# Kernel tuning notes

Measured on AMD Instinct MI355X. Metric: run time of the kernel, lower is better.

The kernel has to match this reference:

```python
import jax, jax.numpy as jnp
import numpy as np

N = 100000   # nodes
E = 1600000  # edges (avg degree 16)
F_IN, F_HID, F_OUT = 64, 64, 16


def setup_inputs() -> dict:
    key = jax.random.key(0)
    ks = jax.random.split(key, 10)
    features = jax.random.normal(ks[0], (N, F_IN), dtype=jnp.float32)
    src = jax.random.randint(ks[1], (E,), 0, N, dtype=jnp.int32)
    dst = jax.random.randint(ks[2], (E,), 0, N, dtype=jnp.int32)
    # Xavier-uniform weights, zero bias (matches nn.init in the module)
    def xavier(k, fan_in, fan_out):
        lim = np.sqrt(6.0 / (fan_in + fan_out))
        return jax.random.uniform(k, (fan_in, fan_out), jnp.float32, -lim, lim)
    return {
        "features": features,
        "W1": xavier(ks[3], F_IN, F_HID), "b1": jnp.zeros((F_HID,), jnp.float32),
        "W2": xavier(ks[4], F_HID, F_HID), "b2": jnp.zeros((F_HID,), jnp.float32),
        "W3": xavier(ks[5], F_HID, F_OUT), "b3": jnp.zeros((F_OUT,), jnp.float32),
        "src": src, "dst": dst,
    }


def pairnorm_scs(x):
    # PairNorm 'PN-SCS', scale=1
    col_mean = x.mean(axis=0)                                    # [F]
    rownorm = jnp.sqrt(1e-6 + jnp.sum(x * x, axis=1, keepdims=True))  # [N,1]
    return x / rownorm - col_mean


def graph_conv(h, src, dst, W, b):
    # copy_u('h','m') + sum reduce over edges, plus self-loop
    agg = jax.ops.segment_sum(h[src], dst, num_segments=N) + h   # [N,F]
    return agg @ W + b


def reference(features, W1, b1, W2, b2, W3, b3, src, dst):
    h = features
    for W, b in ((W1, b1), (W2, b2)):
        h = pairnorm_scs(h)
        h = jax.nn.relu(graph_conv(h, src, dst, W, b))
        # dropout p=0.0 -> identity
    return graph_conv(h, src, dst, W3, b3)
```

## Files before the change

kernel.cpp:

```cpp
#include <hip/hip_runtime.h>
#include <hip/hip_fp8.h>


#define NHB 128

__device__ __forceinline__ unsigned short f2bf(float f) {
  unsigned u = __builtin_bit_cast(unsigned, f);
  u += 0x7FFFu + ((u >> 16) & 1u);
  return (unsigned short)(u >> 16);
}
__device__ __forceinline__ float bf2f(unsigned short h) {
  return __builtin_bit_cast(float, ((unsigned)h) << 16);
}
__device__ __forceinline__ float rlane(float v, int k) {
  return __builtin_bit_cast(
      float, __builtin_amdgcn_readlane(__builtin_bit_cast(int, v), k));
}
__device__ __forceinline__ unsigned char f2fp8(float f) {
  __hip_fp8_e4m3 t(f);
  return (unsigned char)t.__x;
}
__device__ __forceinline__ float fp8tof(unsigned v) {
#if __has_builtin(__builtin_amdgcn_cvt_f32_fp8)
  return __builtin_amdgcn_cvt_f32_fp8((int)v, 0);
#else
  const unsigned h = ((v << 8) & 0x8000u) | ((v << 7) & 0x3f80u);
  __half_raw hr; hr.x = (unsigned short)h;
  return (float)__half(hr) * 256.0f;
#endif
}

__global__ __launch_bounds__(256) void prelude_kernel(
    const int* __restrict__ dst, int* __restrict__ cntA, int E,
    const float* __restrict__ x, float* __restrict__ cs, int n4) {
  __shared__ int lc[NHB];
  __shared__ float lds[16][64];
  const int t = threadIdx.x;
  if (t < NHB) lc[t] = 0;
  __syncthreads();
  const int stride = gridDim.x * blockDim.x;
  for (int e = blockIdx.x * blockDim.x + t; e < E; e += stride)
    atomicAdd(&lc[__builtin_nontemporal_load(&dst[e]) >> 10], 1);

  float s0 = 0.f, s1 = 0.f, s2 = 0.f, s3 = 0.f;
  for (int i = blockIdx.x * blockDim.x + t; i < n4; i += stride) {
    float4 v = ((const float4*)x)[i];
    s0 += v.x; s1 += v.y; s2 += v.z; s3 += v.w;
  }
  const int r = t >> 4;
  const int cq = (t & 15) * 4;
  lds[r][cq + 0] = s0; lds[r][cq + 1] = s1; lds[r][cq + 2] = s2; lds[r][cq + 3] = s3;
  __syncthreads();
  if (t < NHB && lc[t]) atomicAdd(&cntA[t], lc[t]);
  if (t < 64) {
    float tot = 0.f;
    #pragma unroll
    for (int rr = 0; rr < 16; ++rr) tot += lds[rr][t];
    unsafeAtomicAdd(&cs[t], tot);
  }
}

__global__ void colsum_kernel(const float* __restrict__ x, float* __restrict__ cs,
                              int n4) {
  __shared__ float lds[16][64];
  float s0 = 0.f, s1 = 0.f, s2 = 0.f, s3 = 0.f;
  const int t = threadIdx.x;
  const int stride = gridDim.x * blockDim.x;
  for (int i = blockIdx.x * blockDim.x + t; i < n4; i += stride) {
    float4 v = ((const float4*)x)[i];
    s0 += v.x; s1 += v.y; s2 += v.z; s3 += v.w;
  }
  const int r = t >> 4;
  const int cq = (t & 15) * 4;
  lds[r][cq + 0] = s0; lds[r][cq + 1] = s1; lds[r][cq + 2] = s2; lds[r][cq + 3] = s3;
  __syncthreads();
  if (t < 64) {
    float tot = 0.f;
    #pragma unroll
    for (int rr = 0; rr < 16; ++rr) tot += lds[rr][t];
    unsafeAtomicAdd(&cs[t], tot);
  }
}

__global__ __launch_bounds__(256) void matnorm_kernel(
    const float* x, const float* __restrict__ W,
    const float* __restrict__ cs, unsigned char* __restrict__ z,
    int N, float invN) {
  const int lane = threadIdx.x & 63;
  const int wid  = blockIdx.x * (blockDim.x >> 6) + (threadIdx.x >> 6);
  const int nw   = gridDim.x * (blockDim.x >> 6);

  float w[64];
  float cm0 = 0.f, cm1 = 0.f, cm2 = 0.f, cm3 = 0.f;
  #pragma unroll
  for (int k = 0; k < 64; k += 4) {
    w[k + 0] = W[(k + 0) * 64 + lane];
    w[k + 1] = W[(k + 1) * 64 + lane];
    w[k + 2] = W[(k + 2) * 64 + lane];
    w[k + 3] = W[(k + 3) * 64 + lane];
    cm0 = fmaf(cs[k + 0], w[k + 0], cm0);
    cm1 = fmaf(cs[k + 1], w[k + 1], cm1);
    cm2 = fmaf(cs[k + 2], w[k + 2], cm2);
    cm3 = fmaf(cs[k + 3], w[k + 3], cm3);
  }
  const float cm = ((cm0 + cm1) + (cm2 + cm3)) * invN;

  for (int row = wid; row < N; row += nw) {
    const float xv = x[(size_t)row * 64 + lane];
    float ss = xv * xv;
    #pragma unroll
    for (int m = 1; m < 64; m <<= 1) ss += __shfl_xor(ss, m, 64);
    const float rinv = 1.0f / sqrtf(1e-6f + ss);
    float a0 = 0.f, a1 = 0.f, a2 = 0.f, a3 = 0.f;
    #pragma unroll
    for (int k = 0; k < 64; k += 4) {
      a0 = fmaf(rlane(xv, k + 0), w[k + 0], a0);
      a1 = fmaf(rlane(xv, k + 1), w[k + 1], a1);
      a2 = fmaf(rlane(xv, k + 2), w[k + 2], a2);
      a3 = fmaf(rlane(xv, k + 3), w[k + 3], a3);
    }
    const float acc = (a0 + a1) + (a2 + a3);
    z[(size_t)row * 64 + lane] = f2fp8(acc * rinv - cm);
  }
}


__global__ void scanA_kernel(const int* __restrict__ cntA,
                             int* __restrict__ baseA, int* __restrict__ curA,
                             int NHI) {
  if (threadIdx.x == 0) {
    int acc = 0;
    for (int p = 0; p < NHI; ++p) { baseA[p] = acc; curA[p] = acc; acc += cntA[p]; }
    baseA[NHI] = acc;
  }
}

#define TILE 2048
#define CAPA 48
__global__ __launch_bounds__(256) void scatterA_kernel(
    const int* __restrict__ src, const int* __restrict__ dst,
    int* __restrict__ curA, unsigned* __restrict__ ppack, int E) {
  __shared__ unsigned lpk[NHB][CAPA];
  __shared__ int lcnt[NHB], lbase[NHB];
  const int t = threadIdx.x;
  if (t < NHB) lcnt[t] = 0;
  __syncthreads();
  const int ntiles = (E + TILE - 1) / TILE;
  for (int tile = blockIdx.x; tile < ntiles; tile += gridDim.x) {
    const int base = tile * TILE;
    #pragma unroll
    for (int j = 0; j < TILE / 256; ++j) {
      const int e = base + j * 256 + t;
      if (e < E) {
        const int d = __builtin_nontemporal_load(&dst[e]);
        const int s = __builtin_nontemporal_load(&src[e]);
        const unsigned pw = ((unsigned)s << 10) | ((unsigned)d & 1023u);
        const int p = d >> 10;
        const int slot = atomicAdd(&lcnt[p], 1);
        if (slot < CAPA) lpk[p][slot] = pw;
        else ppack[atomicAdd(&curA[p], 1)] = pw;
      }
    }
    __syncthreads();
    if (t < NHB) {
      int c = lcnt[t]; if (c > CAPA) c = CAPA;
      lbase[t] = c ? atomicAdd(&curA[t], c) : 0;
      lcnt[t] = c;
    }
    __syncthreads();
    for (int p = 0; p < NHB; ++p) {
      const int c = lcnt[p];
      if (t < c) ppack[lbase[p] + t] = lpk[p][t];
    }
    __syncthreads();
    if (t < NHB) lcnt[t] = 0;
    __syncthreads();
  }
}

__global__ __launch_bounds__(1024) void fillsort_kernel(
    const unsigned* __restrict__ ppack, const int* __restrict__ baseA,
    int* __restrict__ rowstart, int* __restrict__ csr, int N, int E) {
  __shared__ int hist[1024];
  __shared__ int bs[1024];
  const int t = threadIdx.x;
  const int h = blockIdx.x;
  const int nlo = h << 10;
  const int elo = baseA[h], ehi = baseA[h + 1];

  hist[t] = 0;
  __syncthreads();

  int e = elo + t;
  for (; e + 3 * 1024 < ehi; e += 4 * 1024) {
    const unsigned p0 = ppack[e], p1 = ppack[e + 1024],
                   p2 = ppack[e + 2048], p3 = ppack[e + 3072];
    atomicAdd(&hist[p0 & 1023u], 1); atomicAdd(&hist[p1 & 1023u], 1);
    atomicAdd(&hist[p2 & 1023u], 1); atomicAdd(&hist[p3 & 1023u], 1);
  }
  for (; e < ehi; e += 1024) atomicAdd(&hist[ppack[e] & 1023u], 1);
  __syncthreads();

  const int c = hist[t];
  bs[t] = c;
  __syncthreads();
  for (int off = 1; off < 1024; off <<= 1) {
    const int v = (t >= off) ? bs[t - off] : 0;
    __syncthreads();
    bs[t] += v;
    __syncthreads();
  }
  const int excl = bs[t] - c;

  hist[t] = excl;
  const int n0 = nlo + t;
  if (n0 < N) rowstart[n0] = elo + excl;
  if (h == 0 && t == 0) rowstart[N] = E;
  __syncthreads();

  e = elo + t;
  for (; e + 3 * 1024 < ehi; e += 4 * 1024) {
    const unsigned p0 = ppack[e],        p1 = ppack[e + 1024];
    const unsigned p2 = ppack[e + 2048], p3 = ppack[e + 3072];
    csr[elo + atomicAdd(&hist[p0 & 1023u], 1)] = (int)(p0 >> 10);
    csr[elo + atomicAdd(&hist[p1 & 1023u], 1)] = (int)(p1 >> 10);
    csr[elo + atomicAdd(&hist[p2 & 1023u], 1)] = (int)(p2 >> 10);
    csr[elo + atomicAdd(&hist[p3 & 1023u], 1)] = (int)(p3 >> 10);
  }
  for (; e < ehi; e += 1024) {
    const unsigned p = ppack[e];
    csr[elo + atomicAdd(&hist[p & 1023u], 1)] = (int)(p >> 10);
  }
}

__global__ __launch_bounds__(256) void gather64_kernel(
    const unsigned char* __restrict__ z, const float* __restrict__ b,
    const int* __restrict__ rowstart, const int* __restrict__ csr,
    float* __restrict__ agg, int N) {
  const int lane = threadIdx.x & 63;
  int node = blockIdx.x * (blockDim.x >> 6) + (threadIdx.x >> 6);
  if (node >= N) return;
  node = __builtin_amdgcn_readfirstlane(node);
  const int start = rowstart[node];
  const int end   = rowstart[node + 1];
  const unsigned char hs = z[(size_t)node * 64 + lane];
  float a0 = 0.f, a1 = 0.f, a2 = 0.f, a3 = 0.f;
  int e = start;
  for (; e + 16 <= end; e += 16) {
    unsigned char h[16];
    #pragma unroll
    for (int j = 0; j < 16; ++j) h[j] = z[(size_t)csr[e + j] * 64 + lane];
    #pragma unroll
    for (int j = 0; j < 16; j += 4) {
      a0 += fp8tof(h[j + 0]); a1 += fp8tof(h[j + 1]);
      a2 += fp8tof(h[j + 2]); a3 += fp8tof(h[j + 3]);
    }
  }
  for (; e + 4 <= end; e += 4) {
    unsigned char h[4];
    #pragma unroll
    for (int j = 0; j < 4; ++j) h[j] = z[(size_t)csr[e + j] * 64 + lane];
    a0 += fp8tof(h[0]); a1 += fp8tof(h[1]); a2 += fp8tof(h[2]); a3 += fp8tof(h[3]);
  }
  for (; e < end; ++e) a0 += fp8tof(z[(size_t)csr[e] * 64 + lane]);
  const float sum = (a0 + a1) + (a2 + a3);
  agg[(size_t)node * 64 + lane] = fmaxf(fp8tof(hs) + b[lane] + sum, 0.f);
}

__global__ __launch_bounds__(256) void gather_l2_kernel(
    const unsigned char* __restrict__ z2, const float* __restrict__ b2,
    const float* __restrict__ W3, const int* __restrict__ rowstart,
    const int* __restrict__ csr, unsigned short* __restrict__ z3, int N) {
  const int lane = threadIdx.x & 63;
  int node = blockIdx.x * (blockDim.x >> 6) + (threadIdx.x >> 6);
  if (node >= N) return;
  node = __builtin_amdgcn_readfirstlane(node);
  float4 w4[4];
  #pragma unroll
  for (int q = 0; q < 4; ++q)
    w4[q] = ((const float4*)(W3 + lane * 16))[q];

  const int start = rowstart[node];
  const int end   = rowstart[node + 1];
  const unsigned char hs = z2[(size_t)node * 64 + lane];
  float a0 = 0.f, a1 = 0.f, a2 = 0.f, a3 = 0.f;
  int e = start;
  for (; e + 16 <= end; e += 16) {
    unsigned char h[16];
    #pragma unroll
    for (int j = 0; j < 16; ++j) h[j] = z2[(size_t)csr[e + j] * 64 + lane];
    #pragma unroll
    for (int j = 0; j < 16; j += 4) {
      a0 += fp8tof(h[j + 0]); a1 += fp8tof(h[j + 1]);
      a2 += fp8tof(h[j + 2]); a3 += fp8tof(h[j + 3]);
    }
  }
  for (; e + 4 <= end; e += 4) {
    unsigned char h[4];
    #pragma unroll
    for (int j = 0; j < 4; ++j) h[j] = z2[(size_t)csr[e + j] * 64 + lane];
    a0 += fp8tof(h[0]); a1 += fp8tof(h[1]); a2 += fp8tof(h[2]); a3 += fp8tof(h[3]);
  }
  for (; e < end; ++e) a0 += fp8tof(z2[(size_t)csr[e] * 64 + lane]);
  const float sum = (a0 + a1) + (a2 + a3);
  const float o = fmaxf(fp8tof(hs) + b2[lane] + sum, 0.f);

  float p[16];
  #pragma unroll
  for (int q = 0; q < 4; ++q) {
    p[4 * q + 0] = o * w4[q].x;
    p[4 * q + 1] = o * w4[q].y;
    p[4 * q + 2] = o * w4[q].z;
    p[4 * q + 3] = o * w4[q].w;
  }
  {
    const bool up = (lane & 1);
    #pragma unroll
    for (int m = 0; m < 8; ++m) {
      const float mine = up ? p[m + 8] : p[m];
      const float give = up ? p[m] : p[m + 8];
      p[m] = mine + __shfl_xor(give, 1, 64);
    }
  }
  {
    const bool up = (lane & 2);
    #pragma unroll
    for (int m = 0; m < 4; ++m) {
      const float mine = up ? p[m + 4] : p[m];
      const float give = up ? p[m] : p[m + 4];
      p[m] = mine + __shfl_xor(give, 2, 64);
    }
  }
  {
    const bool up = (lane & 4);
    #pragma unroll
    for (int m = 0; m < 2; ++m) {
      const float mine = up ? p[m + 2] : p[m];
      const float give = up ? p[m] : p[m + 2];
      p[m] = mine + __shfl_xor(give, 4, 64);
    }
  }
  {
    const bool up = (lane & 8);
    const float mine = up ? p[1] : p[0];
    const float give = up ? p[0] : p[1];
    p[0] = mine + __shfl_xor(give, 8, 64);
  }
  p[0] += __shfl_xor(p[0], 16, 64);
  p[0] += __shfl_xor(p[0], 32, 64);

  if (lane < 16) {
    const int j = ((lane & 1) << 3) | ((lane & 2) << 1) |
                  ((lane & 4) >> 1) | ((lane & 8) >> 3);
    z3[(size_t)node * 16 + j] = f2bf(p[0]);
  }
}

__global__ __launch_bounds__(256) void gather16_kernel(
    const unsigned short* __restrict__ z3, const float* __restrict__ b3,
    const int* __restrict__ rowstart, const int* __restrict__ csr,
    float* __restrict__ out, int N) {
  const int lane = threadIdx.x & 63;
  const int f = lane & 15;
  const int g = lane >> 4;
  int node = blockIdx.x * (blockDim.x >> 6) + (threadIdx.x >> 6);
  if (node >= N) return;
  node = __builtin_amdgcn_readfirstlane(node);
  const int start = rowstart[node];
  const int end   = rowstart[node + 1];
  float acc0 = 0.f, acc1 = 0.f;
  int e = start + g;
  for (; e + 4 < end; e += 8) {
    acc0 += bf2f(z3[(size_t)csr[e] * 16 + f]);
    acc1 += bf2f(z3[(size_t)csr[e + 4] * 16 + f]);
  }
  if (e < end) acc0 += bf2f(z3[(size_t)csr[e] * 16 + f]);
  float acc = acc0 + acc1;
  acc += __shfl_xor(acc, 16, 64);
  acc += __shfl_xor(acc, 32, 64);
  if (lane < 16)
    out[(size_t)node * 16 + f] = bf2f(z3[(size_t)node * 16 + f]) + b3[f] + acc;
}

extern "C" void kernel_launch(void* const* d_in, const int* in_sizes, int n_in,
                              void* d_out, int out_size, void* d_ws, size_t ws_size,
                              hipStream_t stream) {
  const float* feat = (const float*)d_in[0];
  const float* W1 = (const float*)d_in[1];
  const float* b1 = (const float*)d_in[2];
  const float* W2 = (const float*)d_in[3];
  const float* b2 = (const float*)d_in[4];
  const float* W3 = (const float*)d_in[5];
  const float* b3 = (const float*)d_in[6];
  const int* src = (const int*)d_in[7];
  const int* dst = (const int*)d_in[8];
  const int N = in_sizes[0] / 64;
  const int E = in_sizes[7];
  float* out = (float*)d_out;

  float* B            = (float*)d_ws;
  unsigned char* zb   = (unsigned char*)(B + (size_t)N * 64);
  unsigned short* z3b = (unsigned short*)(zb + (size_t)N * 64);
  int* cntA  = (int*)(z3b + (size_t)N * 16);
  float* cs1 = (float*)(cntA + NHB);
  float* cs2 = cs1 + 64;
  int* baseA    = (int*)(cs2 + 64);
  int* curA     = baseA + NHB + 1;
  int* rowstart = curA + NHB;
  int* csr      = rowstart + N + 1;
  unsigned* ppack = (unsigned*)zb;

  const int NHI = (N + 1023) >> 10;
  const int node_blocks = (N + 3) / 4;
  const float invN = 1.0f / (float)N;

  hipMemsetAsync(cntA, 0, (NHB + 128) * sizeof(int), stream);
  prelude_kernel<<<512, 256, 0, stream>>>(dst, cntA, E, feat, cs1, N * 16);
  scanA_kernel<<<1, 64, 0, stream>>>(cntA, baseA, curA, NHI);
  scatterA_kernel<<<512, 256, 0, stream>>>(src, dst, curA, ppack, E);
  fillsort_kernel<<<NHI, 1024, 0, stream>>>(ppack, baseA, rowstart, csr, N, E);

  matnorm_kernel<<<1024, 256, 0, stream>>>(feat, W1, cs1, zb, N, invN);
  gather64_kernel<<<node_blocks, 256, 0, stream>>>(zb, b1, rowstart, csr, B, N);

  colsum_kernel<<<512, 256, 0, stream>>>(B, cs2, N * 16);
  matnorm_kernel<<<1024, 256, 0, stream>>>(B, W2, cs2, zb, N, invN);
  gather_l2_kernel<<<node_blocks, 256, 0, stream>>>(zb, b2, W3, rowstart, csr,
                                                    z3b, N);

  gather16_kernel<<<node_blocks, 256, 0, stream>>>(z3b, b3, rowstart, csr, out, N);
}
```

Before: 394.3 us.

## Fuse column sum into layer-1 gather, parallel bucket scan, fp8 final features

Layer 1's gather becomes a grid-stride kernel that also accumulates per-column sums of its ReLU output and adds them atomically. This removes the separate colsum pass over the N×64 float buffer. The single-thread bucket scan becomes a 128-thread shared-memory Hillis-Steele scan. The 16-wide layer-3 projected features are stored as fp8 instead of bf16, halving gather16's read traffic at the cost of precision.

```diff
diff --git a/kernel.cpp b/kernel.cpp
--- a/kernel.cpp
+++ b/kernel.cpp
@@ -52,28 +52,6 @@
   lds[r][cq + 0] = s0; lds[r][cq + 1] = s1; lds[r][cq + 2] = s2; lds[r][cq + 3] = s3;
   __syncthreads();
   if (t < NHB && lc[t]) atomicAdd(&cntA[t], lc[t]);
-  if (t < 64) {
-    float tot = 0.f;
-    #pragma unroll
-    for (int rr = 0; rr < 16; ++rr) tot += lds[rr][t];
-    unsafeAtomicAdd(&cs[t], tot);
-  }
-}
-
-__global__ void colsum_kernel(const float* __restrict__ x, float* __restrict__ cs,
-                              int n4) {
-  __shared__ float lds[16][64];
-  float s0 = 0.f, s1 = 0.f, s2 = 0.f, s3 = 0.f;
-  const int t = threadIdx.x;
-  const int stride = gridDim.x * blockDim.x;
-  for (int i = blockIdx.x * blockDim.x + t; i < n4; i += stride) {
-    float4 v = ((const float4*)x)[i];
-    s0 += v.x; s1 += v.y; s2 += v.z; s3 += v.w;
-  }
-  const int r = t >> 4;
-  const int cq = (t & 15) * 4;
-  lds[r][cq + 0] = s0; lds[r][cq + 1] = s1; lds[r][cq + 2] = s2; lds[r][cq + 3] = s3;
-  __syncthreads();
   if (t < 64) {
     float tot = 0.f;
     #pragma unroll
@@ -128,11 +106,22 @@
 __global__ void scanA_kernel(const int* __restrict__ cntA,
                              int* __restrict__ baseA, int* __restrict__ curA,
                              int NHI) {
-  if (threadIdx.x == 0) {
-    int acc = 0;
-    for (int p = 0; p < NHI; ++p) { baseA[p] = acc; curA[p] = acc; acc += cntA[p]; }
-    baseA[NHI] = acc;
-  }
+  __shared__ int s[NHB];
+  const int t = threadIdx.x;
+  const int v = (t < NHI) ? cntA[t] : 0;
+  s[t] = v;
+  __syncthreads();
+  int acc = v;
+  for (int off = 1; off < NHB; off <<= 1) {
+    const int add = (t >= off) ? s[t - off] : 0;
+    __syncthreads();
+    acc += add;
+    s[t] = acc;
+    __syncthreads();
+  }
+  const int excl = acc - v;
+  if (t < NHI) { baseA[t] = excl; curA[t] = excl; }
+  if (t == NHI - 1) baseA[NHI] = acc;
 }
 
 #define TILE 2048
@@ -236,41 +225,54 @@
 __global__ __launch_bounds__(256) void gather64_kernel(
     const unsigned char* __restrict__ z, const float* __restrict__ b,
     const int* __restrict__ rowstart, const int* __restrict__ csr,
-    float* __restrict__ agg, int N) {
+    float* __restrict__ agg, float* __restrict__ cs, int N) {
+  __shared__ float lred[4][64];
   const int lane = threadIdx.x & 63;
-  int node = blockIdx.x * (blockDim.x >> 6) + (threadIdx.x >> 6);
-  if (node >= N) return;
-  node = __builtin_amdgcn_readfirstlane(node);
-  const int start = rowstart[node];
-  const int end   = rowstart[node + 1];
-  const unsigned char hs = z[(size_t)node * 64 + lane];
-  float a0 = 0.f, a1 = 0.f, a2 = 0.f, a3 = 0.f;
-  int e = start;
-  for (; e + 16 <= end; e += 16) {
-    unsigned char h[16];
-    #pragma unroll
-    for (int j = 0; j < 16; ++j) h[j] = z[(size_t)csr[e + j] * 64 + lane];
-    #pragma unroll
-    for (int j = 0; j < 16; j += 4) {
-      a0 += fp8tof(h[j + 0]); a1 += fp8tof(h[j + 1]);
-      a2 += fp8tof(h[j + 2]); a3 += fp8tof(h[j + 3]);
-    }
-  }
-  for (; e + 4 <= end; e += 4) {
-    unsigned char h[4];
-    #pragma unroll
-    for (int j = 0; j < 4; ++j) h[j] = z[(size_t)csr[e + j] * 64 + lane];
-    a0 += fp8tof(h[0]); a1 += fp8tof(h[1]); a2 += fp8tof(h[2]); a3 += fp8tof(h[3]);
-  }
-  for (; e < end; ++e) a0 += fp8tof(z[(size_t)csr[e] * 64 + lane]);
-  const float sum = (a0 + a1) + (a2 + a3);
-  agg[(size_t)node * 64 + lane] = fmaxf(fp8tof(hs) + b[lane] + sum, 0.f);
+  const int wv   = threadIdx.x >> 6;
+  const int nw   = gridDim.x * (blockDim.x >> 6);
+  const float bl = b[lane];
+  float csum = 0.f;
+  for (int node = blockIdx.x * (blockDim.x >> 6) + wv; node < N; node += nw) {
+    const int n = __builtin_amdgcn_readfirstlane(node);
+    const int start = rowstart[n];
+    const int end   = rowstart[n + 1];
+    const unsigned char hs = z[(size_t)n * 64 + lane];
+    float a0 = 0.f, a1 = 0.f, a2 = 0.f, a3 = 0.f;
+    int e = start;
+    for (; e + 16 <= end; e += 16) {
+      unsigned char h[16];
+      #pragma unroll
+      for (int j = 0; j < 16; ++j) h[j] = z[(size_t)csr[e + j] * 64 + lane];
+      #pragma unroll
+      for (int j = 0; j < 16; j += 4) {
+        a0 += fp8tof(h[j + 0]); a1 += fp8tof(h[j + 1]);
+        a2 += fp8tof(h[j + 2]); a3 += fp8tof(h[j + 3]);
+      }
+    }
+    for (; e + 4 <= end; e += 4) {
+      unsigned char h[4];
+      #pragma unroll
+      for (int j = 0; j < 4; ++j) h[j] = z[(size_t)csr[e + j] * 64 + lane];
+      a0 += fp8tof(h[0]); a1 += fp8tof(h[1]); a2 += fp8tof(h[2]); a3 += fp8tof(h[3]);
+    }
+    for (; e < end; ++e) a0 += fp8tof(z[(size_t)csr[e] * 64 + lane]);
+    const float sum = (a0 + a1) + (a2 + a3);
+    const float o = fmaxf(fp8tof(hs) + bl + sum, 0.f);
+    agg[(size_t)n * 64 + lane] = o;
+    csum += o;
+  }
+  lred[wv][lane] = csum;
+  __syncthreads();
+  if (threadIdx.x < 64) {
+    const float tot = lred[0][lane] + lred[1][lane] + lred[2][lane] + lred[3][lane];
+    unsafeAtomicAdd(&cs[lane], tot);
+  }
 }
 
 __global__ __launch_bounds__(256) void gather_l2_kernel(
     const unsigned char* __restrict__ z2, const float* __restrict__ b2,
     const float* __restrict__ W3, const int* __restrict__ rowstart,
-    const int* __restrict__ csr, unsigned short* __restrict__ z3, int N) {
+    const int* __restrict__ csr, unsigned char* __restrict__ z3, int N) {
   const int lane = threadIdx.x & 63;
   int node = blockIdx.x * (blockDim.x >> 6) + (threadIdx.x >> 6);
   if (node >= N) return;
@@ -352,12 +354,12 @@
   if (lane < 16) {
     const int j = ((lane & 1) << 3) | ((lane & 2) << 1) |
                   ((lane & 4) >> 1) | ((lane & 8) >> 3);
-    z3[(size_t)node * 16 + j] = f2bf(p[0]);
+    z3[(size_t)node * 16 + j] = f2fp8(p[0]);
   }
 }
 
 __global__ __launch_bounds__(256) void gather16_kernel(
-    const unsigned short* __restrict__ z3, const float* __restrict__ b3,
+    const unsigned char* __restrict__ z3, const float* __restrict__ b3,
     const int* __restrict__ rowstart, const int* __restrict__ csr,
     float* __restrict__ out, int N) {
   const int lane = threadIdx.x & 63;
@@ -371,15 +373,15 @@
   float acc0 = 0.f, acc1 = 0.f;
   int e = start + g;
   for (; e + 4 < end; e += 8) {
-    acc0 += bf2f(z3[(size_t)csr[e] * 16 + f]);
-    acc1 += bf2f(z3[(size_t)csr[e + 4] * 16 + f]);
-  }
-  if (e < end) acc0 += bf2f(z3[(size_t)csr[e] * 16 + f]);
+    acc0 += fp8tof(z3[(size_t)csr[e] * 16 + f]);
+    acc1 += fp8tof(z3[(size_t)csr[e + 4] * 16 + f]);
+  }
+  if (e < end) acc0 += fp8tof(z3[(size_t)csr[e] * 16 + f]);
   float acc = acc0 + acc1;
   acc += __shfl_xor(acc, 16, 64);
   acc += __shfl_xor(acc, 32, 64);
   if (lane < 16)
-    out[(size_t)node * 16 + f] = bf2f(z3[(size_t)node * 16 + f]) + b3[f] + acc;
+    out[(size_t)node * 16 + f] = fp8tof(z3[(size_t)node * 16 + f]) + b3[f] + acc;
 }
 
 extern "C" void kernel_launch(void* const* d_in, const int* in_sizes, int n_in,
@@ -400,7 +402,7 @@
 
   float* B            = (float*)d_ws;
   unsigned char* zb   = (unsigned char*)(B + (size_t)N * 64);
-  unsigned short* z3b = (unsigned short*)(zb + (size_t)N * 64);
+  unsigned char* z3b  = zb + (size_t)N * 64;
   int* cntA  = (int*)(z3b + (size_t)N * 16);
   float* cs1 = (float*)(cntA + NHB);
   float* cs2 = cs1 + 64;
@@ -416,14 +418,13 @@
 
   hipMemsetAsync(cntA, 0, (NHB + 128) * sizeof(int), stream);
   prelude_kernel<<<512, 256, 0, stream>>>(dst, cntA, E, feat, cs1, N * 16);
-  scanA_kernel<<<1, 64, 0, stream>>>(cntA, baseA, curA, NHI);
+  scanA_kernel<<<1, NHB, 0, stream>>>(cntA, baseA, curA, NHI);
   scatterA_kernel<<<512, 256, 0, stream>>>(src, dst, curA, ppack, E);
   fillsort_kernel<<<NHI, 1024, 0, stream>>>(ppack, baseA, rowstart, csr, N, E);
 
   matnorm_kernel<<<1024, 256, 0, stream>>>(feat, W1, cs1, zb, N, invN);
-  gather64_kernel<<<node_blocks, 256, 0, stream>>>(zb, b1, rowstart, csr, B, N);
-
-  colsum_kernel<<<512, 256, 0, stream>>>(B, cs2, N * 16);
+  gather64_kernel<<<2048, 256, 0, stream>>>(zb, b1, rowstart, csr, B, cs2, N);
+
   matnorm_kernel<<<1024, 256, 0, stream>>>(B, W2, cs2, zb, N, invN);
   gather_l2_kernel<<<node_blocks, 256, 0, stream>>>(zb, b2, W3, rowstart, csr,
                                                     z3b, N);
```

After: 401.5 us. No clear change (+1.8%).
